# Optimization experiments

Measured on AMD Instinct MI355X. Metric: run time of the kernel, lower is better.

Reference implementation:

```python
import jax, jax.numpy as jnp
import numpy as np

B, C_IN, S = 32, 4, 2048
NF = 256          # CNN filters
H = 256           # LSTM hidden per direction
NH, DH = 8, 64    # heads, single-head size
MH = 512          # multihead size
KSZ, PAD, POOL = 13, 6, 6
SP = (S + 2 * PAD - KSZ + 1) // POOL  # 341: post conv(len-preserving)+maxpool1d length


def _lstm_dir(x, Wih, Whh, b):
    # x: [T, N, C] -- torch LSTM gate order i,f,g,o; b = b_ih + b_hh merged
    N = x.shape[1]
    h0 = jnp.zeros((N, H), x.dtype)
    c0 = jnp.zeros((N, H), x.dtype)

    def step(carry, xt):
        h, c = carry
        g = xt @ Wih.T + h @ Whh.T + b
        i, f, gg, o = jnp.split(g, 4, axis=-1)
        c = jax.nn.sigmoid(f) * c + jax.nn.sigmoid(i) * jnp.tanh(gg)
        h = jax.nn.sigmoid(o) * jnp.tanh(c)
        return (h, c), h

    _, hs = jax.lax.scan(step, (h0, c0), x)
    return hs


def _bilstm(x, Wih, Whh, b):
    fwd = _lstm_dir(x, Wih[0], Whh[0], b[0])
    bwd = _lstm_dir(x[::-1], Wih[1], Whh[1], b[1])[::-1]
    return jnp.concatenate([fwd, bwd], axis=-1)


def _rpe():
    # RelativePosition: |clip(k-q, -(S-1), S-1)| / (S-1); identical across the
    # batch-repeat channels, so compute once then broadcast (same math).
    r = jnp.arange(S)
    d = jnp.abs(jnp.clip(r[None, :] - r[:, None], -(S - 1), S - 1))
    d = d.astype(jnp.float32) / jnp.float32(S - 1)
    # nn.MaxPool2d((9,9), stride=(6,6), padding=1) -> [341, 341]
    return jax.lax.reduce_window(d, -jnp.inf, jax.lax.max, (9, 9), (6, 6), [(1, 1), (1, 1)])


def setup_inputs():
    key = jax.random.key(0)
    ks = jax.random.split(key, 20)
    f = lambda i, shape: jax.random.normal(ks[i], shape, jnp.float32) * 0.05
    return {
        "inputs": jax.random.normal(ks[0], (B, C_IN, S), jnp.float32),
        "conv1_w": f(1, (NF, C_IN, KSZ)),
        "bn1_gamma": jnp.ones((NF,), jnp.float32),
        "bn1_beta": jnp.zeros((NF,), jnp.float32),
        "Wih0": f(2, (2, 4 * H, NF)),
        "Whh0": f(3, (2, 4 * H, H)),
        "b0": f(4, (2, 4 * H)),
        "Wih1": f(5, (2, 4 * H, 2 * H)),
        "Whh1": f(6, (2, 4 * H, H)),
        "b1": f(7, (2, 4 * H)),
        "Qw": f(8, (NH, DH, 2 * H)), "Qb": f(9, (NH, DH)),
        "Kw": f(10, (NH, DH, 2 * H)), "Kb": f(11, (NH, DH)),
        "Vw": f(12, (NH, DH, 2 * H)), "Vb": f(13, (NH, DH)),
        "mh_w": f(14, (MH, NH * DH)), "mh_b": f(15, (MH,)),
    }


def reference(inputs, conv1_w, bn1_gamma, bn1_beta, Wih0, Whh0, b0,
              Wih1, Whh1, b1, Qw, Qb, Kw, Kb, Vw, Vb, mh_w, mh_b):
    # layer1: Conv1d (bias=False, pad=6 keeps length) + BatchNorm1d(eval: mean=0, var=1) + ReLU + MaxPool1d(6)
    x = jax.lax.conv_general_dilated(inputs, conv1_w, (1,), [(PAD, PAD)],
                                     dimension_numbers=('NCH', 'OIH', 'NCH'))
    x = x * (bn1_gamma / jnp.sqrt(1.0 + 1e-5))[None, :, None] + bn1_beta[None, :, None]
    x = jax.nn.relu(x)
    x = jax.lax.reduce_window(x, -jnp.inf, jax.lax.max, (1, 1, POOL), (1, 1, POOL), 'VALID')  # [B,NF,SP]
    x = jnp.transpose(x, (0, 2, 1))  # [B, SP, NF]

    # torch nn.LSTM with batch_first=False fed [B,SP,NF]: scans over axis 0 (batch) -- replicated faithfully.
    x = _bilstm(x, Wih0, Whh0, b0)
    x = _bilstm(x, Wih1, Whh1, b1)  # [B, SP, 2H]
    # (the F_RNN/R_RNN split-and-concat is an identity)

    # per-head Q/K/V (batched over heads), relative attention, dropout off (eval)
    q = jnp.einsum('bsc,hdc->hbsd', x, Qw) + Qb[:, None, None, :]
    k = jnp.einsum('bsc,hdc->hbsd', x, Kw) + Kb[:, None, None, :]
    v = jnp.einsum('bsc,hdc->hbsd', x, Vw) + Vb[:, None, None, :]
    scores = jnp.einsum('hbqd,hbkd->hbqk', q, k) / jnp.sqrt(jnp.float32(DH))
    scores = scores / _rpe()[None, None, :, :]
    p = jax.nn.softmax(scores, axis=-1)
    attn = jax.nn.relu(jnp.einsum('hbqk,hbkd->hbqd', p, v))  # [NH,B,SP,DH]
    cat = jnp.transpose(attn, (1, 2, 0, 3)).reshape(B, SP, NH * DH)
    out = jax.nn.relu(cat @ mh_w.T + mh_b)  # MultiHeadLinear + MHReLU
    return out
```

## Files before the change

### kernel.cpp

```cpp
#include <hip/hip_runtime.h>
#include <math.h>

#define B_    32
#define CIN   4
#define SLEN  2048
#define NF    256
#define HD    256
#define SP    341
#define RTOT  (B_*SP)
#define NH_   8
#define DH_   64
#define GRP   4
#define PSTR  344
#define HS    (SP*HD)

typedef __attribute__((ext_vector_type(8))) short short8;
typedef __attribute__((ext_vector_type(4))) float floatx4;
typedef __attribute__((ext_vector_type(4))) unsigned short ushortx4;
typedef __attribute__((ext_vector_type(8))) unsigned short ushort8;

__device__ __forceinline__ float sigmoidf_(float x) { return 1.0f / (1.0f + expf(-x)); }

__device__ __forceinline__ unsigned short f2bf(float x) {
    unsigned int u = __float_as_uint(x);
    unsigned int r = (u + 0x7FFF + ((u >> 16) & 1)) >> 16;
    return (unsigned short)r;
}
__device__ __forceinline__ float bf2f(unsigned short b) {
    return __uint_as_float(((unsigned int)b) << 16);
}


__global__ __launch_bounds__(256)
void conv_pool_k(const float* __restrict__ in, const float* __restrict__ cw,
                 const float* __restrict__ gamma, const float* __restrict__ beta,
                 unsigned short* __restrict__ x0p)
{
    const int b  = blockIdx.y;
    const int s0 = blockIdx.x * 16;
    const int co = threadIdx.x;
    __shared__ float ins[CIN][16*6 + 12];
    for (int idx = threadIdx.x; idx < CIN*108; idx += 256) {
        int ci = idx / 108, o = idx % 108;
        int pos = 6*s0 - 6 + o;
        ins[ci][o] = (pos >= 0 && pos < SLEN) ? in[(b*CIN + ci)*SLEN + pos] : 0.0f;
    }
    float wreg[52];
    {
        const float4* wp = (const float4*)(cw + co*52);
        #pragma unroll
        for (int j4 = 0; j4 < 13; ++j4) {
            float4 w4 = wp[j4];
            wreg[j4*4+0]=w4.x; wreg[j4*4+1]=w4.y; wreg[j4*4+2]=w4.z; wreg[j4*4+3]=w4.w;
        }
    }
    const float scale = gamma[co] * (1.0f / sqrtf(1.0f + 1e-5f));
    const float shift = beta[co];
    __syncthreads();
    for (int si = 0; si < 16; ++si) {
        int s = s0 + si;
        if (s >= SP) break;
        float win[CIN][18];
        #pragma unroll
        for (int ci = 0; ci < CIN; ++ci)
            #pragma unroll
            for (int o = 0; o < 18; ++o)
                win[ci][o] = ins[ci][6*si + o];
        float m = -1e30f;
        #pragma unroll
        for (int p6 = 0; p6 < 6; ++p6) {
            float acc = 0.0f;
            #pragma unroll
            for (int ci = 0; ci < CIN; ++ci)
                #pragma unroll
                for (int kk = 0; kk < 13; ++kk)
                    acc += win[ci][p6+kk] * wreg[ci*13+kk];
            float val = acc * scale + shift;
            val = fmaxf(val, 0.0f);
            m = fmaxf(m, val);
        }
        unsigned short hb_ = f2bf(m);
        unsigned short lb_ = f2bf(m - bf2f(hb_));
        size_t rb = (size_t)(b*SP + s)*512 + (size_t)(co >> 3)*16 + (co & 7);
        x0p[rb]     = hb_;
        x0p[rb + 8] = lb_;
    }
}

__global__ __launch_bounds__(256)
void pack4_k(const float* __restrict__ W, unsigned short* __restrict__ hi,
             unsigned short* __restrict__ lo, int n4)
{
    int i = blockIdx.x * 256 + threadIdx.x;
    if (i >= n4) return;
    float4 x = *((const float4*)W + i);
    float v[4] = {x.x, x.y, x.z, x.w};
    ushortx4 h, l;
    #pragma unroll
    for (int e = 0; e < 4; ++e) {
        unsigned short hb = f2bf(v[e]);
        h[e] = hb;
        l[e] = f2bf(v[e] - bf2f(hb));
    }
    *((ushortx4*)hi + i) = h;
    *((ushortx4*)lo + i) = l;
}

__global__ __launch_bounds__(256)
void pack8_k(const float* __restrict__ W, unsigned short* __restrict__ O, int n8)
{
    int i = blockIdx.x * 256 + threadIdx.x;
    if (i >= n8) return;
    const float4* wp = (const float4*)W + (size_t)i*2;
    float4 a = wp[0], b = wp[1];
    float v[8] = {a.x,a.y,a.z,a.w,b.x,b.y,b.z,b.w};
    ushort8 h, l;
    #pragma unroll
    for (int e = 0; e < 8; ++e) {
        unsigned short hb = f2bf(v[e]);
        h[e] = hb;
        l[e] = f2bf(v[e] - bf2f(hb));
    }
    *(ushort8*)(O + (size_t)i*16)     = h;
    *(ushort8*)(O + (size_t)i*16 + 8) = l;
}

template<int RELU>
__global__ __launch_bounds__(256)
void gemm_bf_k(const unsigned short* __restrict__ Ap, const unsigned short* __restrict__ Bp,
               const float* __restrict__ bias, float* __restrict__ C,
               int M, int N, int K)
{
    const int n0 = blockIdx.x * 128;
    const int m0 = blockIdx.y * 128;
    const int tid = threadIdx.x;
    const int lane = tid & 63;
    const int w = tid >> 6;
    const int wm = w >> 1, wn = w & 1;
    const int ln15 = lane & 15, lq = lane >> 4;
    const int l8 = lane >> 3, lj = lane & 7;
    const size_t rstr = 2*(size_t)K;

    __shared__ unsigned short As[128*64];
    __shared__ unsigned short Bs[128*64];

    floatx4 acc[4][4];
    #pragma unroll
    for (int i = 0; i < 4; ++i)
        #pragma unroll
        for (int j = 0; j < 4; ++j) acc[i][j] = (floatx4){0.f, 0.f, 0.f, 0.f};

    int rloc[4];
    #pragma unroll
    for (int c = 0; c < 4; ++c) rloc[c] = w*32 + c*8 + l8;
    const int spos = lj ^ (l8 & 7);

    for (int k0 = 0; k0 < K; k0 += 32) {
        short8 va[4], vb[4];
        #pragma unroll
        for (int c = 0; c < 4; ++c) {
            int gra = m0 + rloc[c]; if (gra >= M) gra = M - 1;
            va[c] = *(const short8*)(Ap + (size_t)gra*rstr + k0*2 + lj*8);
            vb[c] = *(const short8*)(Bp + (size_t)(n0 + rloc[c])*rstr + k0*2 + lj*8);
        }
        __syncthreads();
        #pragma unroll
        for (int c = 0; c < 4; ++c) {
            *(short8*)&As[rloc[c]*64 + spos*8] = va[c];
            *(short8*)&Bs[rloc[c]*64 + spos*8] = vb[c];
        }
        __syncthreads();

        short8 fa_h[4], fa_l[4], fb_h[4], fb_l[4];
        #pragma unroll
        for (int mt = 0; mt < 4; ++mt) {
            const int lr = wm*64 + mt*16 + ln15;
            fa_h[mt] = *(const short8*)&As[lr*64 + (((lq*2  ) ^ (lr&7))*8)];
            fa_l[mt] = *(const short8*)&As[lr*64 + (((lq*2+1) ^ (lr&7))*8)];
        }
        #pragma unroll
        for (int nt = 0; nt < 4; ++nt) {
            const int lr = wn*64 + nt*16 + ln15;
            fb_h[nt] = *(const short8*)&Bs[lr*64 + (((lq*2  ) ^ (lr&7))*8)];
            fb_l[nt] = *(const short8*)&Bs[lr*64 + (((lq*2+1) ^ (lr&7))*8)];
        }
        #pragma unroll
        for (int mt = 0; mt < 4; ++mt)
            #pragma unroll
            for (int nt = 0; nt < 4; ++nt) {
                acc[mt][nt] = __builtin_amdgcn_mfma_f32_16x16x32_bf16(fa_l[mt], fb_h[nt], acc[mt][nt], 0, 0, 0);
                acc[mt][nt] = __builtin_amdgcn_mfma_f32_16x16x32_bf16(fa_h[mt], fb_l[nt], acc[mt][nt], 0, 0, 0);
                acc[mt][nt] = __builtin_amdgcn_mfma_f32_16x16x32_bf16(fa_h[mt], fb_h[nt], acc[mt][nt], 0, 0, 0);
            }
    }

    #pragma unroll
    for (int nt = 0; nt < 4; ++nt) {
        const int n = n0 + wn*64 + nt*16 + ln15;
        const float bv = bias[n];
        #pragma unroll
        for (int mt = 0; mt < 4; ++mt) {
            const int mbase = m0 + wm*64 + mt*16 + lq*4;
            #pragma unroll
            for (int r = 0; r < 4; ++r) {
                int m = mbase + r;
                if (m < M) {
                    float val = acc[mt][nt][r] + bv;
                    if (RELU) val = fmaxf(val, 0.0f);
                    C[(size_t)m*N + n] = val;
                }
            }
        }
    }
}

__global__ __launch_bounds__(256)
void lstm_step_mfma_k(const float* __restrict__ G,
                      const unsigned short* __restrict__ Whi,
                      const unsigned short* __restrict__ Wlo,
                      const float* __restrict__ h_in,
                      float* __restrict__ h_out,
                      float* __restrict__ c_st,
                      unsigned short* __restrict__ x_out,
                      int s)
{
    const int j0 = blockIdx.x * 32;
    const int m0 = blockIdx.y * 32;
    const int d  = blockIdx.z;
    const int t_in = d ? (B_ - 1 - s) : s;
    const int tid = threadIdx.x;
    const int w = tid >> 6, lane = tid & 63;
    const int mhalf = w & 1, gpair = w >> 1;
    const int ln15 = lane & 15, lq = lane >> 4;

    __shared__ float Csh[32][132];

    int am = m0 + mhalf*16 + ln15; if (am > SP-1) am = SP-1;
    const int akoff = lq * 8;
    const float* hA = h_in + (size_t)d*HS + (size_t)am*HD;

    const unsigned short* WhiD = Whi + (size_t)d*1024*256;
    const unsigned short* WloD = Wlo + (size_t)d*1024*256;
    int nrow[4];
    #pragma unroll
    for (int t = 0; t < 4; ++t)
        nrow[t] = (gpair*2 + (t>>1))*256 + j0 + (t&1)*16 + ln15;

    floatx4 acc[4];
    #pragma unroll
    for (int t = 0; t < 4; ++t) acc[t] = (floatx4){0.f, 0.f, 0.f, 0.f};

    #pragma unroll
    for (int kk = 0; kk < 8; ++kk) {
        const int ko = kk*32 + akoff;
        float4 v0 = *(const float4*)(hA + ko);
        float4 v1 = *(const float4*)(hA + ko + 4);
        float vv[8] = {v0.x, v0.y, v0.z, v0.w, v1.x, v1.y, v1.z, v1.w};
        short8 ahi, alo;
        #pragma unroll
        for (int e = 0; e < 8; ++e) {
            unsigned short hb16 = f2bf(vv[e]);
            ahi[e] = (short)hb16;
            alo[e] = (short)f2bf(vv[e] - bf2f(hb16));
        }
        #pragma unroll
        for (int t = 0; t < 4; ++t) {
            short8 bhi = *(const short8*)(WhiD + (size_t)nrow[t]*HD + ko);
            short8 blo = *(const short8*)(WloD + (size_t)nrow[t]*HD + ko);
            acc[t] = __builtin_amdgcn_mfma_f32_16x16x32_bf16(alo, bhi, acc[t], 0, 0, 0);
            acc[t] = __builtin_amdgcn_mfma_f32_16x16x32_bf16(ahi, blo, acc[t], 0, 0, 0);
            acc[t] = __builtin_amdgcn_mfma_f32_16x16x32_bf16(ahi, bhi, acc[t], 0, 0, 0);
        }
    }

    #pragma unroll
    for (int t = 0; t < 4; ++t) {
        int col = gpair*64 + (t>>1)*32 + (t&1)*16 + ln15;
        int rb  = mhalf*16 + lq*4;
        #pragma unroll
        for (int r = 0; r < 4; ++r)
            Csh[rb + r][col] = acc[t][r];
    }
    __syncthreads();

    const int emloc = tid >> 3;
    const int ej4   = (tid & 7) * 4;
    const int em    = m0 + emloc;
    if (em < SP) {
        size_t gb = ((size_t)t_in*SP + em)*2048 + (size_t)d*1024 + j0 + ej4;
        float4 gi4 = *(const float4*)&G[gb];
        float4 gf4 = *(const float4*)&G[gb + 256];
        float4 gg4 = *(const float4*)&G[gb + 512];
        float4 go4 = *(const float4*)&G[gb + 768];
        size_t cbase = ((size_t)d*SP + em)*HD + j0 + ej4;
        float4 cold = *(float4*)&c_st[cbase];
        float hv[4];
        #pragma unroll
        for (int e = 0; e < 4; ++e) {
            float gi = Csh[emloc][     ej4+e] + (&gi4.x)[e];
            float gf = Csh[emloc][32 + ej4+e] + (&gf4.x)[e];
            float gg = Csh[emloc][64 + ej4+e] + (&gg4.x)[e];
            float go = Csh[emloc][96 + ej4+e] + (&go4.x)[e];
            float cn = sigmoidf_(gf)*(&cold.x)[e] + sigmoidf_(gi)*tanhf(gg);
            (&cold.x)[e] = cn;
            hv[e] = sigmoidf_(go)*tanhf(cn);
        }
        *(float4*)&c_st[cbase] = cold;
        float4 ho; ho.x = hv[0]; ho.y = hv[1]; ho.z = hv[2]; ho.w = hv[3];
        *(float4*)&h_out[cbase] = ho;
        const int colg = d*HD + j0 + ej4;
        size_t xb = ((size_t)t_in*SP + em)*1024 + (size_t)(colg >> 3)*16 + (colg & 7);
        ushortx4 xh, xl;
        #pragma unroll
        for (int e = 0; e < 4; ++e) {
            unsigned short hb16 = f2bf(hv[e]);
            xh[e] = hb16;
            xl[e] = f2bf(hv[e] - bf2f(hb16));
        }
        *(ushortx4*)&x_out[xb]     = xh;
        *(ushortx4*)&x_out[xb + 8] = xl;
    }
}

__global__ __launch_bounds__(256)
void scores_k(const float* __restrict__ q, const float* __restrict__ k,
              float* __restrict__ P, int g)
{
    const int h = blockIdx.z, bl = blockIdx.y, bg = g*GRP + bl;
    const int q0 = (blockIdx.x / 6) * 64;
    const int k0 = (blockIdx.x % 6) * 64;
    const int tid = threadIdx.x;
    __shared__ float qs[64][68];
    __shared__ float ks[64][68];
    {
        int jr = tid >> 2, c16 = (tid & 3) * 16;
        int qq = q0 + jr; if (qq > SP-1) qq = SP-1;
        int kr = k0 + jr; if (kr > SP-1) kr = SP-1;
        const float* qp = &q[((size_t)bg*SP + qq)*512 + h*64 + c16];
        const float* kp = &k[((size_t)bg*SP + kr)*512 + h*64 + c16];
        #pragma unroll
        for (int u = 0; u < 4; ++u) {
            *(float4*)&qs[jr][c16 + u*4] = *(const float4*)(qp + u*4);
            *(float4*)&ks[jr][c16 + u*4] = *(const float4*)(kp + u*4);
        }
    }
    __syncthreads();
    const int tx = tid & 15, ty = tid >> 4;
    float acc[4][4];
    #pragma unroll
    for (int i = 0; i < 4; ++i)
        #pragma unroll
        for (int j = 0; j < 4; ++j) acc[i][j] = 0.0f;
    for (int d4 = 0; d4 < 64; d4 += 4) {
        float4 a[4], b[4];
        #pragma unroll
        for (int i = 0; i < 4; ++i) a[i] = *(const float4*)&qs[ty + 16*i][d4];
        #pragma unroll
        for (int j = 0; j < 4; ++j) b[j] = *(const float4*)&ks[tx + 16*j][d4];
        #pragma unroll
        for (int i = 0; i < 4; ++i)
            #pragma unroll
            for (int j = 0; j < 4; ++j)
                acc[i][j] += a[i].x*b[j].x + a[i].y*b[j].y + a[i].z*b[j].z + a[i].w*b[j].w;
    }
    #pragma unroll
    for (int i = 0; i < 4; ++i) {
        int qq = q0 + ty + 16*i;
        if (qq >= SP) continue;
        int r0 = 6*qq - 1; if (r0 < 0) r0 = 0;
        int r1 = 6*qq + 7; if (r1 > SLEN-1) r1 = SLEN-1;
        size_t rowb = ((size_t)(h*GRP + bl)*SP + qq) * PSTR;
        #pragma unroll
        for (int j = 0; j < 4; ++j) {
            int kk = k0 + tx + 16*j;
            if (kk >= SP) continue;
            int c0 = 6*kk - 1; if (c0 < 0) c0 = 0;
            int c1 = 6*kk + 7;
            int dd1 = c1 - r0; if (dd1 < 0) dd1 = -dd1;
            int dd2 = r1 - c0; if (dd2 < 0) dd2 = -dd2;
            int den = dd1 > dd2 ? dd1 : dd2;
            P[rowb + kk] = (acc[i][j] * 0.125f) * 2047.0f / (float)den;
        }
    }
}

__global__ __launch_bounds__(256)
void softmax_k(float* __restrict__ P)
{
    const int tid = threadIdx.x;
    const int row = blockIdx.x * 4 + (tid >> 6);
    const int lane = tid & 63;
    float* rp = P + (size_t)row * PSTR;
    float v[6];
    float m = -1e30f;
    #pragma unroll
    for (int i = 0; i < 6; ++i) {
        int col = lane + 64*i;
        v[i] = (col < SP) ? rp[col] : -1e30f;
        m = fmaxf(m, v[i]);
    }
    #pragma unroll
    for (int o = 1; o < 64; o <<= 1) m = fmaxf(m, __shfl_xor(m, o, 64));
    float s = 0.0f;
    #pragma unroll
    for (int i = 0; i < 6; ++i) {
        v[i] = expf(v[i] - m);
        s += v[i];
    }
    #pragma unroll
    for (int o = 1; o < 64; o <<= 1) s += __shfl_xor(s, o, 64);
    float inv = 1.0f / s;
    #pragma unroll
    for (int i = 0; i < 6; ++i) {
        int col = lane + 64*i;
        if (col < SP) rp[col] = v[i] * inv;
    }
}

__global__ __launch_bounds__(256)
void pv_k(const float* __restrict__ P, const float* __restrict__ v,
          unsigned short* __restrict__ catp, int g)
{
    const int h = blockIdx.z, bl = blockIdx.y, bg = g*GRP + bl;
    const int q0 = blockIdx.x * 64;
    const int tid = threadIdx.x;
    __shared__ float ps[64][68];
    __shared__ float vs[64][68];
    const int tx = tid & 15, ty = tid >> 4;
    float acc[4][4];
    #pragma unroll
    for (int i = 0; i < 4; ++i)
        #pragma unroll
        for (int j = 0; j < 4; ++j) acc[i][j] = 0.0f;

    for (int kc = 0; kc < 6; ++kc) {
        const int kk0 = kc * 64;
        {
            int jr = tid >> 2, c16 = (tid & 3) * 16;
            int qq = q0 + jr; if (qq > SP-1) qq = SP-1;
            const float* pp = P + ((size_t)(h*GRP + bl)*SP + qq)*PSTR + kk0 + c16;
            #pragma unroll
            for (int u = 0; u < 4; ++u) {
                float4 w = *(const float4*)(pp + u*4);
                int klb = c16 + u*4;
                float vals[4] = {w.x, w.y, w.z, w.w};
                #pragma unroll
                for (int e = 0; e < 4; ++e)
                    ps[klb + e][jr] = (kk0 + klb + e < SP) ? vals[e] : 0.0f;
            }
        }
        {
            int jr = tid >> 2, c16 = (tid & 3) * 16;
            int kr = kk0 + jr; if (kr > SP-1) kr = SP-1;
            const float* vp = &v[((size_t)bg*SP + kr)*512 + h*64 + c16];
            #pragma unroll
            for (int u = 0; u < 4; ++u)
                *(float4*)&vs[jr][c16 + u*4] = *(const float4*)(vp + u*4);
        }
        __syncthreads();
        for (int kk = 0; kk < 64; ++kk) {
            float4 a4 = *(const float4*)&ps[kk][ty*4];
            float4 b4 = *(const float4*)&vs[kk][tx*4];
            float av[4] = {a4.x, a4.y, a4.z, a4.w};
            float bv[4] = {b4.x, b4.y, b4.z, b4.w};
            #pragma unroll
            for (int i = 0; i < 4; ++i)
                #pragma unroll
                for (int j = 0; j < 4; ++j)
                    acc[i][j] += av[i] * bv[j];
        }
        __syncthreads();
    }
    #pragma unroll
    for (int i = 0; i < 4; ++i) {
        int qq = q0 + ty*4 + i;
        if (qq >= SP) continue;
        float r[4];
        r[0] = fmaxf(acc[i][0], 0.0f);
        r[1] = fmaxf(acc[i][1], 0.0f);
        r[2] = fmaxf(acc[i][2], 0.0f);
        r[3] = fmaxf(acc[i][3], 0.0f);
        const int colg = h*64 + tx*4;
        size_t xb = ((size_t)bg*SP + qq)*1024 + (size_t)(colg >> 3)*16 + (colg & 7);
        ushortx4 xh, xl;
        #pragma unroll
        for (int e = 0; e < 4; ++e) {
            unsigned short hb16 = f2bf(r[e]);
            xh[e] = hb16;
            xl[e] = f2bf(r[e] - bf2f(hb16));
        }
        *(ushortx4*)&catp[xb]     = xh;
        *(ushortx4*)&catp[xb + 8] = xl;
    }
}

extern "C" void kernel_launch(void* const* d_in, const int* in_sizes, int n_in,
                              void* d_out, int out_size, void* d_ws, size_t ws_size,
                              hipStream_t stream)
{
    (void)in_sizes; (void)n_in; (void)out_size; (void)ws_size;
    const float* in    = (const float*)d_in[0];
    const float* cw    = (const float*)d_in[1];
    const float* gamma = (const float*)d_in[2];
    const float* beta  = (const float*)d_in[3];
    const float* Wih0  = (const float*)d_in[4];
    const float* Whh0  = (const float*)d_in[5];
    const float* b0    = (const float*)d_in[6];
    const float* Wih1  = (const float*)d_in[7];
    const float* Whh1  = (const float*)d_in[8];
    const float* b1    = (const float*)d_in[9];
    const float* Qw    = (const float*)d_in[10];
    const float* Qb    = (const float*)d_in[11];
    const float* Kw    = (const float*)d_in[12];
    const float* Kb    = (const float*)d_in[13];
    const float* Vw    = (const float*)d_in[14];
    const float* Vb    = (const float*)d_in[15];
    const float* mhw   = (const float*)d_in[16];
    const float* mhb   = (const float*)d_in[17];
    float* out = (float*)d_out;

    float* x0 = (float*)d_ws;
    float* G  = x0 + (size_t)RTOT*NF;
    float* x1 = G  + (size_t)RTOT*2048;
    float* x2 = x1 + (size_t)RTOT*512;
    float* hb = x2 + (size_t)RTOT*512;
    float* cb = hb + (size_t)2*2*SP*HD;

    float* qbuf = G;
    float* kbuf = G + (size_t)RTOT*512;
    float* vbuf = G + (size_t)2*RTOT*512;
    float* P    = G + (size_t)3*RTOT*512;
    const size_t hsz = (size_t)2*SP*HD;

    unsigned short* x0p = (unsigned short*)x0;
    unsigned short* whh1_hi = (unsigned short*)x0;
    unsigned short* whh1_lo = whh1_hi + (size_t)524288;
    unsigned short* wih0_p  = (unsigned short*)x2;
    unsigned short* wih1_p  = wih0_p + (size_t)1048576;
    unsigned short* whh0_hi = wih1_p + (size_t)2097152;
    unsigned short* whh0_lo = whh0_hi + (size_t)524288;
    unsigned short* x1p  = (unsigned short*)x1;
    unsigned short* catp = (unsigned short*)x1;
    unsigned short* x2p = (unsigned short*)x2;
    float* gslack = P + (size_t)NH_*GRP*SP*PSTR;
    unsigned short* qw_p = (unsigned short*)gslack;
    unsigned short* kw_p = qw_p + (size_t)524288;
    unsigned short* vw_p = kw_p + (size_t)524288;
    unsigned short* mw_p = vw_p + (size_t)524288;

    #define PACKGRID(n) dim3(((n) + 255) / 256)

    conv_pool_k<<<dim3(22, B_), 256, 0, stream>>>(in, cw, gamma, beta, x0p);
    pack8_k<<<PACKGRID(65536), 256, 0, stream>>>(Wih0, wih0_p, 65536);
    gemm_bf_k<0><<<dim3(16, 86), 256, 0, stream>>>(x0p, wih0_p, b0, G, RTOT, 2048, 256);
    pack4_k<<<PACKGRID(131072), 256, 0, stream>>>(Whh0, whh0_hi, whh0_lo, 131072);
    pack4_k<<<PACKGRID(131072), 256, 0, stream>>>(Whh1, whh1_hi, whh1_lo, 131072);
    pack8_k<<<PACKGRID(131072), 256, 0, stream>>>(Wih1, wih1_p, 131072);
    hipMemsetAsync(hb, 0, 2*hsz*sizeof(float), stream);
    hipMemsetAsync(cb, 0, hsz*sizeof(float), stream);
    for (int s = 0; s < B_; ++s) {
        float* hin  = hb + (size_t)(s & 1) * hsz;
        float* hout = hb + (size_t)((s+1) & 1) * hsz;
        lstm_step_mfma_k<<<dim3(8, 11, 2), 256, 0, stream>>>(
            G, whh0_hi, whh0_lo, hin, hout, cb, x1p, s);
    }
    gemm_bf_k<0><<<dim3(16, 86), 256, 0, stream>>>(x1p, wih1_p, b1, G, RTOT, 2048, 512);
    hipMemsetAsync(hb, 0, 2*hsz*sizeof(float), stream);
    hipMemsetAsync(cb, 0, hsz*sizeof(float), stream);
    for (int s = 0; s < B_; ++s) {
        float* hin  = hb + (size_t)(s & 1) * hsz;
        float* hout = hb + (size_t)((s+1) & 1) * hsz;
        lstm_step_mfma_k<<<dim3(8, 11, 2), 256, 0, stream>>>(
            G, whh1_hi, whh1_lo, hin, hout, cb, x2p, s);
    }
    pack8_k<<<PACKGRID(32768), 256, 0, stream>>>(Qw,  qw_p, 32768);
    pack8_k<<<PACKGRID(32768), 256, 0, stream>>>(Kw,  kw_p, 32768);
    pack8_k<<<PACKGRID(32768), 256, 0, stream>>>(Vw,  vw_p, 32768);
    pack8_k<<<PACKGRID(32768), 256, 0, stream>>>(mhw, mw_p, 32768);
    gemm_bf_k<0><<<dim3(4, 86), 256, 0, stream>>>(x2p, qw_p, Qb, qbuf, RTOT, 512, 512);
    gemm_bf_k<0><<<dim3(4, 86), 256, 0, stream>>>(x2p, kw_p, Kb, kbuf, RTOT, 512, 512);
    gemm_bf_k<0><<<dim3(4, 86), 256, 0, stream>>>(x2p, vw_p, Vb, vbuf, RTOT, 512, 512);
    for (int g = 0; g < B_/GRP; ++g) {
        scores_k <<<dim3(36, GRP, NH_), 256, 0, stream>>>(qbuf, kbuf, P, g);
        softmax_k<<<dim3(NH_*GRP*SP/4), 256, 0, stream>>>(P);
        pv_k     <<<dim3(6, GRP, NH_), 256, 0, stream>>>(P, vbuf, catp, g);
    }
    gemm_bf_k<1><<<dim3(4, 86), 256, 0, stream>>>(catp, mw_p, mhb, out, RTOT, 512, 512);
    #undef PACKGRID
}
```

Baseline: 1.693 ms.

## Fuse LSTM timestep launches into one persistent cooperative kernel with grid sync

Replaces the 32 per-timestep LSTM kernel launches per layer with a single cooperative kernel that loops over timesteps and uses grid.sync between steps. It also drops the h/c memsets by skipping the recurrent matmul and zeroing the cell state at step 0. This targets launch overhead and the gaps between many small dependent kernels, at the cost of grid-wide barrier latency and requiring all 176 blocks to be co-resident.

New measurement: 2.999 ms. +77.2%, slower.

```diff
diff --git a/kernel.cpp b/kernel.cpp
--- a/kernel.cpp
+++ b/kernel.cpp
@@ -1,5 +1,8 @@
 #include <hip/hip_runtime.h>
+#include <hip/hip_cooperative_groups.h>
 #include <math.h>
+
+namespace cg = cooperative_groups;
 
 #define B_    32
 #define CIN   4
@@ -215,29 +218,27 @@
 }
 
 __global__ __launch_bounds__(256)
-void lstm_step_mfma_k(const float* __restrict__ G,
-                      const unsigned short* __restrict__ Whi,
-                      const unsigned short* __restrict__ Wlo,
-                      const float* __restrict__ h_in,
-                      float* __restrict__ h_out,
-                      float* __restrict__ c_st,
-                      unsigned short* __restrict__ x_out,
-                      int s)
-{
+void lstm_scan_k(const float* __restrict__ G,
+                 const unsigned short* __restrict__ Whi,
+                 const unsigned short* __restrict__ Wlo,
+                 float* __restrict__ hb,
+                 float* __restrict__ c_st,
+                 unsigned short* __restrict__ x_out)
+{
+    cg::grid_group grid = cg::this_grid();
     const int j0 = blockIdx.x * 32;
     const int m0 = blockIdx.y * 32;
     const int d  = blockIdx.z;
-    const int t_in = d ? (B_ - 1 - s) : s;
     const int tid = threadIdx.x;
     const int w = tid >> 6, lane = tid & 63;
     const int mhalf = w & 1, gpair = w >> 1;
     const int ln15 = lane & 15, lq = lane >> 4;
+    const size_t hsz = (size_t)2*SP*HD;
 
     __shared__ float Csh[32][132];
 
     int am = m0 + mhalf*16 + ln15; if (am > SP-1) am = SP-1;
     const int akoff = lq * 8;
-    const float* hA = h_in + (size_t)d*HS + (size_t)am*HD;
 
     const unsigned short* WhiD = Whi + (size_t)d*1024*256;
     const unsigned short* WloD = Wlo + (size_t)d*1024*256;
@@ -246,79 +247,91 @@
     for (int t = 0; t < 4; ++t)
         nrow[t] = (gpair*2 + (t>>1))*256 + j0 + (t&1)*16 + ln15;
 
-    floatx4 acc[4];
-    #pragma unroll
-    for (int t = 0; t < 4; ++t) acc[t] = (floatx4){0.f, 0.f, 0.f, 0.f};
-
-    #pragma unroll
-    for (int kk = 0; kk < 8; ++kk) {
-        const int ko = kk*32 + akoff;
-        float4 v0 = *(const float4*)(hA + ko);
-        float4 v1 = *(const float4*)(hA + ko + 4);
-        float vv[8] = {v0.x, v0.y, v0.z, v0.w, v1.x, v1.y, v1.z, v1.w};
-        short8 ahi, alo;
-        #pragma unroll
-        for (int e = 0; e < 8; ++e) {
-            unsigned short hb16 = f2bf(vv[e]);
-            ahi[e] = (short)hb16;
-            alo[e] = (short)f2bf(vv[e] - bf2f(hb16));
-        }
-        #pragma unroll
-        for (int t = 0; t < 4; ++t) {
-            short8 bhi = *(const short8*)(WhiD + (size_t)nrow[t]*HD + ko);
-            short8 blo = *(const short8*)(WloD + (size_t)nrow[t]*HD + ko);
-            acc[t] = __builtin_amdgcn_mfma_f32_16x16x32_bf16(alo, bhi, acc[t], 0, 0, 0);
-            acc[t] = __builtin_amdgcn_mfma_f32_16x16x32_bf16(ahi, blo, acc[t], 0, 0, 0);
-            acc[t] = __builtin_amdgcn_mfma_f32_16x16x32_bf16(ahi, bhi, acc[t], 0, 0, 0);
-        }
-    }
-
-    #pragma unroll
-    for (int t = 0; t < 4; ++t) {
-        int col = gpair*64 + (t>>1)*32 + (t&1)*16 + ln15;
-        int rb  = mhalf*16 + lq*4;
-        #pragma unroll
-        for (int r = 0; r < 4; ++r)
-            Csh[rb + r][col] = acc[t][r];
-    }
-    __syncthreads();
-
     const int emloc = tid >> 3;
     const int ej4   = (tid & 7) * 4;
     const int em    = m0 + emloc;
-    if (em < SP) {
-        size_t gb = ((size_t)t_in*SP + em)*2048 + (size_t)d*1024 + j0 + ej4;
-        float4 gi4 = *(const float4*)&G[gb];
-        float4 gf4 = *(const float4*)&G[gb + 256];
-        float4 gg4 = *(const float4*)&G[gb + 512];
-        float4 go4 = *(const float4*)&G[gb + 768];
-        size_t cbase = ((size_t)d*SP + em)*HD + j0 + ej4;
-        float4 cold = *(float4*)&c_st[cbase];
-        float hv[4];
-        #pragma unroll
-        for (int e = 0; e < 4; ++e) {
-            float gi = Csh[emloc][     ej4+e] + (&gi4.x)[e];
-            float gf = Csh[emloc][32 + ej4+e] + (&gf4.x)[e];
-            float gg = Csh[emloc][64 + ej4+e] + (&gg4.x)[e];
-            float go = Csh[emloc][96 + ej4+e] + (&go4.x)[e];
-            float cn = sigmoidf_(gf)*(&cold.x)[e] + sigmoidf_(gi)*tanhf(gg);
-            (&cold.x)[e] = cn;
-            hv[e] = sigmoidf_(go)*tanhf(cn);
-        }
-        *(float4*)&c_st[cbase] = cold;
-        float4 ho; ho.x = hv[0]; ho.y = hv[1]; ho.z = hv[2]; ho.w = hv[3];
-        *(float4*)&h_out[cbase] = ho;
-        const int colg = d*HD + j0 + ej4;
-        size_t xb = ((size_t)t_in*SP + em)*1024 + (size_t)(colg >> 3)*16 + (colg & 7);
-        ushortx4 xh, xl;
-        #pragma unroll
-        for (int e = 0; e < 4; ++e) {
-            unsigned short hb16 = f2bf(hv[e]);
-            xh[e] = hb16;
-            xl[e] = f2bf(hv[e] - bf2f(hb16));
-        }
-        *(ushortx4*)&x_out[xb]     = xh;
-        *(ushortx4*)&x_out[xb + 8] = xl;
+
+    for (int s = 0; s < B_; ++s) {
+        const int t_in = d ? (B_ - 1 - s) : s;
+        const float* hA = hb + (size_t)(s & 1)*hsz + (size_t)d*HS + (size_t)am*HD;
+        float* h_out = hb + (size_t)((s+1) & 1)*hsz;
+
+        floatx4 acc[4];
+        #pragma unroll
+        for (int t = 0; t < 4; ++t) acc[t] = (floatx4){0.f, 0.f, 0.f, 0.f};
+
+        if (s > 0) {
+            #pragma unroll
+            for (int kk = 0; kk < 8; ++kk) {
+                const int ko = kk*32 + akoff;
+                float4 v0 = *(const float4*)(hA + ko);
+                float4 v1 = *(const float4*)(hA + ko + 4);
+                float vv[8] = {v0.x, v0.y, v0.z, v0.w, v1.x, v1.y, v1.z, v1.w};
+                short8 ahi, alo;
+                #pragma unroll
+                for (int e = 0; e < 8; ++e) {
+                    unsigned short hb16 = f2bf(vv[e]);
+                    ahi[e] = (short)hb16;
+                    alo[e] = (short)f2bf(vv[e] - bf2f(hb16));
+                }
+                #pragma unroll
+                for (int t = 0; t < 4; ++t) {
+                    short8 bhi = *(const short8*)(WhiD + (size_t)nrow[t]*HD + ko);
+                    short8 blo = *(const short8*)(WloD + (size_t)nrow[t]*HD + ko);
+                    acc[t] = __builtin_amdgcn_mfma_f32_16x16x32_bf16(alo, bhi, acc[t], 0, 0, 0);
+                    acc[t] = __builtin_amdgcn_mfma_f32_16x16x32_bf16(ahi, blo, acc[t], 0, 0, 0);
+                    acc[t] = __builtin_amdgcn_mfma_f32_16x16x32_bf16(ahi, bhi, acc[t], 0, 0, 0);
+                }
+            }
+        }
+
+        #pragma unroll
+        for (int t = 0; t < 4; ++t) {
+            int col = gpair*64 + (t>>1)*32 + (t&1)*16 + ln15;
+            int rb  = mhalf*16 + lq*4;
+            #pragma unroll
+            for (int r = 0; r < 4; ++r)
+                Csh[rb + r][col] = acc[t][r];
+        }
+        __syncthreads();
+
+        if (em < SP) {
+            size_t gb = ((size_t)t_in*SP + em)*2048 + (size_t)d*1024 + j0 + ej4;
+            float4 gi4 = *(const float4*)&G[gb];
+            float4 gf4 = *(const float4*)&G[gb + 256];
+            float4 gg4 = *(const float4*)&G[gb + 512];
+            float4 go4 = *(const float4*)&G[gb + 768];
+            size_t cbase = ((size_t)d*SP + em)*HD + j0 + ej4;
+            float4 cold;
+            if (s > 0) cold = *(float4*)&c_st[cbase];
+            else       cold = (float4){0.f, 0.f, 0.f, 0.f};
+            float hv[4];
+            #pragma unroll
+            for (int e = 0; e < 4; ++e) {
+                float gi = Csh[emloc][     ej4+e] + (&gi4.x)[e];
+                float gf = Csh[emloc][32 + ej4+e] + (&gf4.x)[e];
+                float gg = Csh[emloc][64 + ej4+e] + (&gg4.x)[e];
+                float go = Csh[emloc][96 + ej4+e] + (&go4.x)[e];
+                float cn = sigmoidf_(gf)*(&cold.x)[e] + sigmoidf_(gi)*tanhf(gg);
+                (&cold.x)[e] = cn;
+                hv[e] = sigmoidf_(go)*tanhf(cn);
+            }
+            *(float4*)&c_st[cbase] = cold;
+            float4 ho; ho.x = hv[0]; ho.y = hv[1]; ho.z = hv[2]; ho.w = hv[3];
+            *(float4*)&h_out[cbase] = ho;
+            const int colg = d*HD + j0 + ej4;
+            size_t xb = ((size_t)t_in*SP + em)*1024 + (size_t)(colg >> 3)*16 + (colg & 7);
+            ushortx4 xh, xl;
+            #pragma unroll
+            for (int e = 0; e < 4; ++e) {
+                unsigned short hb16 = f2bf(hv[e]);
+                xh[e] = hb16;
+                xl[e] = f2bf(hv[e] - bf2f(hb16));
+            }
+            *(ushortx4*)&x_out[xb]     = xh;
+            *(ushortx4*)&x_out[xb + 8] = xl;
+        }
+        grid.sync();
     }
 }
 
@@ -530,7 +543,6 @@
     float* kbuf = G + (size_t)RTOT*512;
     float* vbuf = G + (size_t)2*RTOT*512;
     float* P    = G + (size_t)3*RTOT*512;
-    const size_t hsz = (size_t)2*SP*HD;
 
     unsigned short* x0p = (unsigned short*)x0;
     unsigned short* whh1_hi = (unsigned short*)x0;
@@ -556,22 +568,18 @@
     pack4_k<<<PACKGRID(131072), 256, 0, stream>>>(Whh0, whh0_hi, whh0_lo, 131072);
     pack4_k<<<PACKGRID(131072), 256, 0, stream>>>(Whh1, whh1_hi, whh1_lo, 131072);
     pack8_k<<<PACKGRID(131072), 256, 0, stream>>>(Wih1, wih1_p, 131072);
-    hipMemsetAsync(hb, 0, 2*hsz*sizeof(float), stream);
-    hipMemsetAsync(cb, 0, hsz*sizeof(float), stream);
-    for (int s = 0; s < B_; ++s) {
-        float* hin  = hb + (size_t)(s & 1) * hsz;
-        float* hout = hb + (size_t)((s+1) & 1) * hsz;
-        lstm_step_mfma_k<<<dim3(8, 11, 2), 256, 0, stream>>>(
-            G, whh0_hi, whh0_lo, hin, hout, cb, x1p, s);
+    {
+        const float* a0 = G; const unsigned short* a1 = whh0_hi; const unsigned short* a2 = whh0_lo;
+        float* a3 = hb; float* a4 = cb; unsigned short* a5 = x1p;
+        void* kargs[] = {&a0, &a1, &a2, &a3, &a4, &a5};
+        hipLaunchCooperativeKernel((void*)lstm_scan_k, dim3(8, 11, 2), dim3(256, 1, 1), kargs, 0, stream);
     }
     gemm_bf_k<0><<<dim3(16, 86), 256, 0, stream>>>(x1p, wih1_p, b1, G, RTOT, 2048, 512);
-    hipMemsetAsync(hb, 0, 2*hsz*sizeof(float), stream);
-    hipMemsetAsync(cb, 0, hsz*sizeof(float), stream);
-    for (int s = 0; s < B_; ++s) {
-        float* hin  = hb + (size_t)(s & 1) * hsz;
-        float* hout = hb + (size_t)((s+1) & 1) * hsz;
-        lstm_step_mfma_k<<<dim3(8, 11, 2), 256, 0, stream>>>(
-            G, whh1_hi, whh1_lo, hin, hout, cb, x2p, s);
+    {
+        const float* a0 = G; const unsigned short* a1 = whh1_hi; const unsigned short* a2 = whh1_lo;
+        float* a3 = hb; float* a4 = cb; unsigned short* a5 = x2p;
+        void* kargs[] = {&a0, &a1, &a2, &a3, &a4, &a5};
+        hipLaunchCooperativeKernel((void*)lstm_scan_k, dim3(8, 11, 2), dim3(256, 1, 1), kargs, 0, stream);
     }
     pack8_k<<<PACKGRID(32768), 256, 0, stream>>>(Qw,  qw_p, 32768);
     pack8_k<<<PACKGRID(32768), 256, 0, stream>>>(Kw,  kw_p, 32768);
```
